# Optimization experiments

Measured on AMD Instinct MI355X. Metric: run time of the kernel, lower is better.

Reference implementation:

```python
import jax, jax.numpy as jnp
import numpy as np
import math

D_MODEL = 1024
D_STATE = 64
DT_MIN, DT_MAX = 1e-3, 1e-1


def setup_inputs() -> dict:
    key = jax.random.key(0)
    ks = jax.random.split(key, 8)
    x = jax.random.normal(ks[0], (2, 4096, D_MODEL), dtype=jnp.float32)
    # in_proj / out_proj: nn.Linear default init (kaiming-uniform-ish); uniform is fine for a reference
    lim = 1.0 / math.sqrt(D_MODEL)
    Win = jax.random.uniform(ks[1], (D_MODEL, D_MODEL), minval=-lim, maxval=lim, dtype=jnp.float32)
    bin_ = jax.random.uniform(ks[2], (D_MODEL,), minval=-lim, maxval=lim, dtype=jnp.float32)
    Wout = jax.random.uniform(ks[3], (D_MODEL, D_MODEL), minval=-lim, maxval=lim, dtype=jnp.float32)
    bout = jax.random.uniform(ks[4], (D_MODEL,), minval=-lim, maxval=lim, dtype=jnp.float32)
    # HiPPO-LegS style init: A_log[d, n] = log(n + 1)
    A_log = jnp.broadcast_to(jnp.log(jnp.arange(1, D_STATE + 1, dtype=jnp.float32)), (D_MODEL, D_STATE))
    B = 0.1 * jax.random.normal(ks[5], (D_MODEL, D_STATE), dtype=jnp.float32)
    C = 0.1 * jax.random.normal(ks[6], (D_MODEL, D_STATE), dtype=jnp.float32)
    Dp = jnp.ones((D_MODEL,), dtype=jnp.float32)
    log_dt = jax.random.uniform(ks[7], (D_MODEL,), dtype=jnp.float32) * (math.log(DT_MAX) - math.log(DT_MIN)) + math.log(DT_MIN)
    dt = jnp.exp(log_dt)
    return {"x": x, "Win": Win, "bin_": bin_, "A_log": A_log, "B": B, "C": C,
            "Dp": Dp, "dt": dt, "Wout": Wout, "bout": bout}


def reference(x, Win, bin_, A_log, B, C, Dp, dt, Wout, bout):
    b, L, d = x.shape
    x = x @ Win.T + bin_                      # in_proj
    u = jnp.transpose(x, (0, 2, 1))           # [b, d, l]
    A = -jnp.exp(-A_log)                      # [d, n], negative real poles
    logdA = A * dt[:, None]                   # log(dA) since dA = exp(A*dt) > 0
    dB = B * dt[:, None]                      # [d, n]
    t = jnp.arange(L, dtype=x.dtype)
    # dA**t == exp(t * log dA): vectorized Vandermonde, replaces per-step power loop
    powers = jnp.exp(logdA[:, :, None] * t)   # [d, n, L]
    k = jnp.einsum('dn,dnl->dl', C * dB, powers)  # SSM conv kernel [d, L]
    n_fft = 2 * L
    k_f = jnp.fft.rfft(k, n=n_fft)            # [d, F]
    u_f = jnp.fft.rfft(u, n=n_fft)            # [b, d, F]
    y = jnp.fft.irfft(u_f * k_f[None], n=n_fft)[..., :L]  # causal conv
    y = y + u * Dp[:, None]                   # skip connection
    y = jnp.transpose(y, (0, 2, 1))           # [b, l, d]
    return y @ Wout.T + bout                  # out_proj
```

## Files before the change

### kernel.cpp

```cpp
#include <hip/hip_runtime.h>
#include <cstdint>
#include <cstddef>

#define D_MODEL 1024
#define D_STATE 64
#define SEQ     4096
#define BATCH   2
#define MROWS   (BATCH*SEQ)

typedef __bf16 bf16x8 __attribute__((ext_vector_type(8)));
typedef float  f32x4  __attribute__((ext_vector_type(4)));
typedef unsigned short u16;
typedef unsigned int   u32;

union BF8 { bf16x8 v; uint4 q; u16 e[8]; };

__device__ __forceinline__ u16 f2bf(float x) {
    u32 u = __float_as_uint(x);
    u32 r = u + 0x7FFFu + ((u >> 16) & 1u);
    return (u16)(r >> 16);
}
__device__ __forceinline__ float bf2f(u16 h) {
    return __uint_as_float(((u32)h) << 16);
}
__device__ __forceinline__ uint4 pack8u(const u16* e) {
    return make_uint4((u32)e[0] | ((u32)e[1] << 16), (u32)e[2] | ((u32)e[3] << 16),
                      (u32)e[4] | ((u32)e[5] << 16), (u32)e[6] | ((u32)e[7] << 16));
}

__device__ __forceinline__ void async16(const void* g, void* l) {
    __builtin_amdgcn_global_load_lds(
        (const __attribute__((address_space(1))) unsigned int*)(uintptr_t)g,
        (__attribute__((address_space(3))) unsigned int*)(uintptr_t)l,
        16, 0, 0);
}

__global__ __launch_bounds__(256) void prep_kernel(
    const float* __restrict__ x, const float* __restrict__ Win,
    const float* __restrict__ Wout,
    u16* __restrict__ Ax, u16* __restrict__ Bw1, u16* __restrict__ Bw2)
{
    const int blk = blockIdx.x, tid = threadIdx.x;
    const int k = tid * 4;
    const float* src; u16* dst; int row;
    if (blk < MROWS)                  { src = x;    dst = Ax;  row = blk; }
    else if (blk < MROWS + D_MODEL)   { src = Win;  dst = Bw1; row = blk - MROWS; }
    else                              { src = Wout; dst = Bw2; row = blk - MROWS - D_MODEL; }
    const float4 v = *reinterpret_cast<const float4*>(src + (size_t)row * D_MODEL + k);
    *reinterpret_cast<uint2*>(dst + (size_t)row * D_MODEL + k) =
        make_uint2((u32)f2bf(v.x) | ((u32)f2bf(v.y) << 16),
                   (u32)f2bf(v.z) | ((u32)f2bf(v.w) << 16));
}

template<int MODE>
__global__ __launch_bounds__(256) void gemm_bt(
    const u16* __restrict__ A, const u16* __restrict__ Bm,
    const float* __restrict__ bias, float* __restrict__ out)
{
    __shared__ u16 As[128 * 64];
    __shared__ u16 Bs[128 * 64];
    __shared__ float Tt[MODE == 1 ? 4 * 16 * 65 : 4];
    const int m0 = blockIdx.y * 128, n0 = blockIdx.x * 128;
    const int tid = threadIdx.x;
    const int wave = tid >> 6, lane = tid & 63;
    const int wm = wave >> 1, wn = wave & 1;
    const int qm = lane & 15, qk = lane >> 4;
    f32x4 acc[4][4] = {};
    for (int k0 = 0; k0 < D_MODEL; k0 += 64) {
        #pragma unroll
        for (int it = 0; it < 4; ++it) {
            const int c   = it * 256 + tid;
            const int row = c >> 3, col = (c & 7) * 8;
            const int ldsbase = (it * 256 + wave * 64) * 8;
            async16(&A[(size_t)(m0 + row) * D_MODEL + k0 + col], &As[ldsbase]);
            async16(&Bm[(size_t)(n0 + row) * D_MODEL + k0 + col], &Bs[ldsbase]);
        }
        __syncthreads();
        #pragma unroll
        for (int kk = 0; kk < 2; ++kk) {
            bf16x8 af[4], bg[4];
            #pragma unroll
            for (int i = 0; i < 4; ++i) {
                af[i] = *reinterpret_cast<const bf16x8*>(&As[(wm*64 + i*16 + qm)*64 + kk*32 + qk*8]);
                bg[i] = *reinterpret_cast<const bf16x8*>(&Bs[(wn*64 + i*16 + qm)*64 + kk*32 + qk*8]);
            }
            #pragma unroll
            for (int i = 0; i < 4; ++i)
                #pragma unroll
                for (int j = 0; j < 4; ++j)
                    acc[i][j] = __builtin_amdgcn_mfma_f32_16x16x32_bf16(af[i], bg[j], acc[i][j], 0, 0, 0);
        }
        __syncthreads();
    }
    if (MODE == 0) {
        #pragma unroll
        for (int i = 0; i < 4; ++i) {
            const int r0 = m0 + wm*64 + i*16 + qk*4;
            #pragma unroll
            for (int j = 0; j < 4; ++j) {
                const int c = n0 + wn*64 + j*16 + qm;
                const float bv = bias[c];
                #pragma unroll
                for (int reg = 0; reg < 4; ++reg)
                    out[(size_t)(r0 + reg) * D_MODEL + c] = acc[i][j][reg] + bv;
            }
        }
    } else {
        float* T = &Tt[wave * 16 * 65];
        float bvj[4];
        #pragma unroll
        for (int j = 0; j < 4; ++j) bvj[j] = bias[n0 + wn*64 + j*16 + qm];
        const int dcol = n0 + wn*64 + lane;
        #pragma unroll
        for (int i = 0; i < 4; ++i) {
            #pragma unroll
            for (int j = 0; j < 4; ++j)
                #pragma unroll
                for (int reg = 0; reg < 4; ++reg)
                    T[(qk*4 + reg) * 65 + j*16 + qm] = acc[i][j][reg] + bvj[j];
            __builtin_amdgcn_wave_barrier();
            float4 o[4];
            #pragma unroll
            for (int t4 = 0; t4 < 4; ++t4)
                o[t4] = make_float4(T[(t4*4 + 0) * 65 + lane], T[(t4*4 + 1) * 65 + lane],
                                    T[(t4*4 + 2) * 65 + lane], T[(t4*4 + 3) * 65 + lane]);
            const int r0 = m0 + wm*64 + i*16;
            const int bb = r0 >> 12, l0 = r0 & (SEQ - 1);
            float* dst = &out[((size_t)(bb * D_MODEL + dcol)) * SEQ + l0];
            #pragma unroll
            for (int t4 = 0; t4 < 4; ++t4)
                reinterpret_cast<float4*>(dst)[t4] = o[t4];
            __builtin_amdgcn_wave_barrier();
        }
    }
}

__global__ __launch_bounds__(128) void scan2_kernel(
    float* __restrict__ ut, const float* __restrict__ A_log,
    const float* __restrict__ Bp, const float* __restrict__ Cp,
    const float* __restrict__ dtp, const float* __restrict__ Dpv)
{
    __shared__ u16 KT_s[64 * 72];
    __shared__ u16 RA_s[64 * 72];
    __shared__ u16 P2_s[64 * 72];
    __shared__ u16 SH[2][64 * 72];
    const int d = blockIdx.x, tid = threadIdx.x;
    const int w = tid >> 6, lane = tid & 63;
    const int qm = lane & 15, qk = lane >> 4;

    const float dt_d  = dtp[d];
    const float logdA = -expf(-A_log[d * D_STATE + lane]) * dt_d;
    const float r     = expf(logdA);
    const float dBn   = Bp[d * D_STATE + lane] * dt_d;
    const float Cv    = Cp[d * D_STATE + lane];
    const float rTn   = expf(logdA * 64.0f);
    const float Dpd   = Dpv[d];

    float* ug = ut + ((size_t)(w * D_MODEL + d)) * SEQ;

    bf16x8 Uf[4][4];
    #pragma unroll
    for (int ct = 0; ct < 4; ++ct) {
        const float* src = ug + (ct * 16 + qm) * 64;
        #pragma unroll
        for (int jb = 0; jb < 2; ++jb) {
            const float4 v0 = *reinterpret_cast<const float4*>(src + jb * 32 + qk * 8);
            const float4 v1 = *reinterpret_cast<const float4*>(src + jb * 32 + qk * 8 + 4);
            const float fv[8] = {v0.x, v0.y, v0.z, v0.w, v1.x, v1.y, v1.z, v1.w};
            BF8 hi, lo;
            #pragma unroll
            for (int i = 0; i < 8; ++i) {
                hi.e[i] = f2bf(fv[i]);
                lo.e[i] = f2bf(fv[i] - bf2f(hi.e[i]));
            }
            Uf[ct][jb]     = hi.v;
            Uf[ct][jb + 2] = lo.v;
        }
    }

    if (w == 1) {
        {
            float p = Cv;
            for (int t = 0; t < 64; ++t) { p *= r; P2_s[t * 72 + lane] = f2bf(p); }
        }
        {
            for (int o = 0; o < 8; ++o) {
                float tmp[8];
                tmp[7] = expf(logdA * (float)(63 - (o * 8 + 7)));
                #pragma unroll
                for (int i = 6; i >= 0; --i) tmp[i] = tmp[i + 1] * r;
                u16 e[8];
                #pragma unroll
                for (int i = 0; i < 8; ++i) e[i] = f2bf(tmp[i]);
                *reinterpret_cast<uint4*>(&RA_s[lane * 72 + o * 8]) = pack8u(e);
            }
        }
    } else {
        float* scr = reinterpret_cast<float*>(&SH[0][0]);
        float* ksh = scr + 64 * 65;
        {
            float p = Cv * dBn;
            for (int m = 0; m < 64; ++m) { scr[m * 65 + lane] = p; p *= r; }
        }
        {
            float kacc = 0.f;
            for (int n = 0; n < 64; ++n) kacc += scr[lane * 65 + n];
            ksh[lane] = kacc;
        }
        {
            for (int o = 0; o < 8; ++o) {
                u16 e[8];
                #pragma unroll
                for (int i = 0; i < 8; ++i) {
                    const int j = o * 8 + i;
                    e[i] = (j <= lane) ? f2bf(ksh[lane - j]) : (u16)0;
                }
                *reinterpret_cast<uint4*>(&KT_s[lane * 72 + o * 8]) = pack8u(e);
            }
        }
    }
    __syncthreads();

    u16* sh = SH[w];
    {
        bf16x8 Af[4][2];
        #pragma unroll
        for (int nt = 0; nt < 4; ++nt)
            #pragma unroll
            for (int jb = 0; jb < 2; ++jb)
                Af[nt][jb] = *reinterpret_cast<const bf16x8*>(
                    &RA_s[(nt * 16 + qm) * 72 + jb * 32 + qk * 8]);
        f32x4 acc[4][4] = {};
        #pragma unroll
        for (int kk = 0; kk < 4; ++kk)
            #pragma unroll
            for (int nt = 0; nt < 4; ++nt)
                #pragma unroll
                for (int ct = 0; ct < 4; ++ct)
                    acc[nt][ct] = __builtin_amdgcn_mfma_f32_16x16x32_bf16(
                        Af[nt][kk & 1], Uf[ct][kk], acc[nt][ct], 0, 0, 0);
        #pragma unroll
        for (int nt = 0; nt < 4; ++nt)
            #pragma unroll
            for (int ct = 0; ct < 4; ++ct) {
                const int c = ct * 16 + qm, nn0 = nt * 16 + qk * 4;
                uint2 pk;
                pk.x = (u32)f2bf(acc[nt][ct][0]) | ((u32)f2bf(acc[nt][ct][1]) << 16);
                pk.y = (u32)f2bf(acc[nt][ct][2]) | ((u32)f2bf(acc[nt][ct][3]) << 16);
                *reinterpret_cast<uint2*>(&sh[c * 72 + nn0]) = pk;
            }
    }
    __syncthreads();

    {
        float h = 0.f;
        for (int c = 0; c < 64; ++c) {
            const float s = bf2f(sh[c * 72 + lane]);
            sh[c * 72 + lane] = f2bf(h);
            h = rTn * h + dBn * s;
        }
    }
    __syncthreads();

    {
        bf16x8 Af[4][2];
        #pragma unroll
        for (int tt = 0; tt < 4; ++tt)
            #pragma unroll
            for (int jb = 0; jb < 2; ++jb)
                Af[tt][jb] = *reinterpret_cast<const bf16x8*>(
                    &KT_s[(tt * 16 + qm) * 72 + jb * 32 + qk * 8]);
        f32x4 acc[4][4] = {};
        #pragma unroll
        for (int kk = 0; kk < 4; ++kk)
            #pragma unroll
            for (int tt = 0; tt < 4; ++tt)
                #pragma unroll
                for (int ct = 0; ct < 4; ++ct)
                    acc[tt][ct] = __builtin_amdgcn_mfma_f32_16x16x32_bf16(
                        Af[tt][kk & 1], Uf[ct][kk], acc[tt][ct], 0, 0, 0);
        bf16x8 Pf[4][2];
        #pragma unroll
        for (int tt = 0; tt < 4; ++tt)
            #pragma unroll
            for (int kb = 0; kb < 2; ++kb)
                Pf[tt][kb] = *reinterpret_cast<const bf16x8*>(
                    &P2_s[(tt * 16 + qm) * 72 + kb * 32 + qk * 8]);
        #pragma unroll
        for (int ct = 0; ct < 4; ++ct)
            #pragma unroll
            for (int kb = 0; kb < 2; ++kb) {
                const bf16x8 Hf = *reinterpret_cast<const bf16x8*>(
                    &sh[(ct * 16 + qm) * 72 + kb * 32 + qk * 8]);
                #pragma unroll
                for (int tt = 0; tt < 4; ++tt)
                    acc[tt][ct] = __builtin_amdgcn_mfma_f32_16x16x32_bf16(
                        Pf[tt][kb], Hf, acc[tt][ct], 0, 0, 0);
            }
        #pragma unroll
        for (int tt = 0; tt < 4; ++tt)
            #pragma unroll
            for (int ct = 0; ct < 4; ++ct) {
                const int c = ct * 16 + qm, t0 = tt * 16 + qk * 4;
                float* dst = ug + c * 64 + t0;
                const float4 u4 = *reinterpret_cast<const float4*>(dst);
                float4 y;
                y.x = acc[tt][ct][0] + Dpd * u4.x;
                y.y = acc[tt][ct][1] + Dpd * u4.y;
                y.z = acc[tt][ct][2] + Dpd * u4.z;
                y.w = acc[tt][ct][3] + Dpd * u4.w;
                *reinterpret_cast<float4*>(dst) = y;
            }
    }
}

__global__ __launch_bounds__(256) void trans_kernel(
    const float* __restrict__ yt, u16* __restrict__ Ax)
{
    __shared__ float T[64 * 68];
    const int b = blockIdx.z, dx = blockIdx.y * 64, lx = blockIdx.x * 64;
    const int tid = threadIdx.x;
    const int t16 = tid >> 4, l16 = tid & 15;
    #pragma unroll
    for (int ii = 0; ii < 4; ++ii) {
        const int dd = ii * 16 + t16;
        const int ll = l16 * 4;
        float4 v = *reinterpret_cast<const float4*>(
            &yt[((size_t)(b * D_MODEL + dx + dd)) * SEQ + lx + ll]);
        *reinterpret_cast<float4*>(&T[dd * 68 + ll]) = v;
    }
    __syncthreads();
    #pragma unroll
    for (int ii = 0; ii < 4; ++ii) {
        const int ll = ii * 16 + t16;
        const int dd = l16 * 4;
        float v0 = T[(dd + 0) * 68 + ll], v1 = T[(dd + 1) * 68 + ll];
        float v2 = T[(dd + 2) * 68 + ll], v3 = T[(dd + 3) * 68 + ll];
        const size_t row = (size_t)b * SEQ + lx + ll;
        *reinterpret_cast<uint2*>(Ax + row * D_MODEL + dx + dd) =
            make_uint2((u32)f2bf(v0) | ((u32)f2bf(v1) << 16),
                       (u32)f2bf(v2) | ((u32)f2bf(v3) << 16));
    }
}

extern "C" void kernel_launch(void* const* d_in, const int* in_sizes, int n_in,
                              void* d_out, int out_size, void* d_ws, size_t ws_size,
                              hipStream_t stream) {
    const float* x     = (const float*)d_in[0];
    const float* Win   = (const float*)d_in[1];
    const float* bin   = (const float*)d_in[2];
    const float* A_log = (const float*)d_in[3];
    const float* Bp    = (const float*)d_in[4];
    const float* Cp    = (const float*)d_in[5];
    const float* Dpv   = (const float*)d_in[6];
    const float* dtp   = (const float*)d_in[7];
    const float* Wout  = (const float*)d_in[8];
    const float* bout  = (const float*)d_in[9];
    float* out = (float*)d_out;

    char* ws = (char*)d_ws;
    u16*   Ax  = (u16*)(ws);
    float* ut  = (float*)(ws + (size_t)25165824);
    u16*   Bw1 = (u16*)(ws + (size_t)58720256);
    u16*   Bw2 = (u16*)(ws + (size_t)60817408);

    prep_kernel<<<MROWS + 2 * D_MODEL, 256, 0, stream>>>(x, Win, Wout, Ax, Bw1, Bw2);
    gemm_bt<1><<<dim3(D_MODEL / 128, MROWS / 128), 256, 0, stream>>>(Ax, Bw1, bin, ut);
    scan2_kernel<<<D_MODEL, 128, 0, stream>>>(ut, A_log, Bp, Cp, dtp, Dpv);
    trans_kernel<<<dim3(SEQ / 64, D_MODEL / 64, BATCH), 256, 0, stream>>>(ut, Ax);
    gemm_bt<0><<<dim3(D_MODEL / 128, MROWS / 128), 256, 0, stream>>>(Ax, Bw2, bout, out);
}
```

Measured before the change: 199.1 us.

## Double-buffer GEMM LDS tiles and restructure SSM kernel precompute

The GEMM now uses two LDS buffers so the async global loads for the next K-slice overlap MFMA work on the current one, with one barrier per slice instead of two. The transpose scratch for MODE 1 reuses the A tile buffer. In the scan kernel, the SSM kernel taps are computed as a dot product of dB with the bf16 power table instead of a 64x65 fp32 scratch, the precompute work is rebalanced across the two waves, and the LDS row stride drops from 72 to 64. The sequential state recurrence batches its LDS reads in groups of 16. Dropping the padding may add LDS bank conflicts, and computing k from bf16 powers costs some precision.

```diff
diff --git a/kernel.cpp b/kernel.cpp
--- a/kernel.cpp
+++ b/kernel.cpp
@@ -57,32 +57,33 @@
     const u16* __restrict__ A, const u16* __restrict__ Bm,
     const float* __restrict__ bias, float* __restrict__ out)
 {
-    __shared__ u16 As[128 * 64];
-    __shared__ u16 Bs[128 * 64];
-    __shared__ float Tt[MODE == 1 ? 4 * 16 * 65 : 4];
+    __shared__ __align__(16) u16 As[2][128 * 64];
+    __shared__ __align__(16) u16 Bs[2][128 * 64];
     const int m0 = blockIdx.y * 128, n0 = blockIdx.x * 128;
     const int tid = threadIdx.x;
     const int wave = tid >> 6, lane = tid & 63;
     const int wm = wave >> 1, wn = wave & 1;
     const int qm = lane & 15, qk = lane >> 4;
     f32x4 acc[4][4] = {};
-    for (int k0 = 0; k0 < D_MODEL; k0 += 64) {
+
+    auto stage = [&](u16* Ad, u16* Bd, int k0) {
         #pragma unroll
         for (int it = 0; it < 4; ++it) {
             const int c   = it * 256 + tid;
             const int row = c >> 3, col = (c & 7) * 8;
             const int ldsbase = (it * 256 + wave * 64) * 8;
-            async16(&A[(size_t)(m0 + row) * D_MODEL + k0 + col], &As[ldsbase]);
-            async16(&Bm[(size_t)(n0 + row) * D_MODEL + k0 + col], &Bs[ldsbase]);
-        }
-        __syncthreads();
+            async16(&A[(size_t)(m0 + row) * D_MODEL + k0 + col], Ad + ldsbase);
+            async16(&Bm[(size_t)(n0 + row) * D_MODEL + k0 + col], Bd + ldsbase);
+        }
+    };
+    auto compute = [&](const u16* As_, const u16* Bs_) {
         #pragma unroll
         for (int kk = 0; kk < 2; ++kk) {
             bf16x8 af[4], bg[4];
             #pragma unroll
             for (int i = 0; i < 4; ++i) {
-                af[i] = *reinterpret_cast<const bf16x8*>(&As[(wm*64 + i*16 + qm)*64 + kk*32 + qk*8]);
-                bg[i] = *reinterpret_cast<const bf16x8*>(&Bs[(wn*64 + i*16 + qm)*64 + kk*32 + qk*8]);
+                af[i] = *reinterpret_cast<const bf16x8*>(&As_[(wm*64 + i*16 + qm)*64 + kk*32 + qk*8]);
+                bg[i] = *reinterpret_cast<const bf16x8*>(&Bs_[(wn*64 + i*16 + qm)*64 + kk*32 + qk*8]);
             }
             #pragma unroll
             for (int i = 0; i < 4; ++i)
@@ -90,8 +91,24 @@
                 for (int j = 0; j < 4; ++j)
                     acc[i][j] = __builtin_amdgcn_mfma_f32_16x16x32_bf16(af[i], bg[j], acc[i][j], 0, 0, 0);
         }
+    };
+
+    stage(As[0], Bs[0], 0);
+    __syncthreads();
+    #pragma unroll 1
+    for (int kp = 0; kp < 7; ++kp) {
+        stage(As[1], Bs[1], 128 * kp + 64);
+        compute(As[0], Bs[0]);
         __syncthreads();
-    }
+        stage(As[0], Bs[0], 128 * kp + 128);
+        compute(As[1], Bs[1]);
+        __syncthreads();
+    }
+    stage(As[1], Bs[1], 960);
+    compute(As[0], Bs[0]);
+    __syncthreads();
+    compute(As[1], Bs[1]);
+
     if (MODE == 0) {
         #pragma unroll
         for (int i = 0; i < 4; ++i) {
@@ -106,6 +123,7 @@
             }
         }
     } else {
+        float* Tt = reinterpret_cast<float*>(&As[0][0]);
         float* T = &Tt[wave * 16 * 65];
         float bvj[4];
         #pragma unroll
@@ -140,10 +158,10 @@
     const float* __restrict__ Bp, const float* __restrict__ Cp,
     const float* __restrict__ dtp, const float* __restrict__ Dpv)
 {
-    __shared__ u16 KT_s[64 * 72];
-    __shared__ u16 RA_s[64 * 72];
-    __shared__ u16 P2_s[64 * 72];
-    __shared__ u16 SH[2][64 * 72];
+    __shared__ __align__(16) u16 KT_s[64 * 64];
+    __shared__ __align__(16) u16 RA_s[64 * 64];
+    __shared__ __align__(16) u16 P2_s[64 * 64];
+    __shared__ __align__(16) u16 SH[2][64 * 64];
     const int d = blockIdx.x, tid = threadIdx.x;
     const int w = tid >> 6, lane = tid & 63;
     const int qm = lane & 15, qk = lane >> 4;
@@ -158,6 +176,10 @@
 
     float* ug = ut + ((size_t)(w * D_MODEL + d)) * SEQ;
 
+    float* dB_sh = reinterpret_cast<float*>(&SH[0][0]);
+    float* w_sh  = dB_sh + 64;
+    float* k_sh  = dB_sh + 128;
+
     bf16x8 Uf[4][4];
     #pragma unroll
     for (int ct = 0; ct < 4; ++ct) {
@@ -178,45 +200,45 @@
         }
     }
 
-    if (w == 1) {
-        {
-            float p = Cv;
-            for (int t = 0; t < 64; ++t) { p *= r; P2_s[t * 72 + lane] = f2bf(p); }
-        }
-        {
+    if (w == 0) {
+        dB_sh[lane] = dBn;
+        w_sh[lane]  = Cv * dBn;
+        for (int o = 0; o < 8; ++o) {
+            float tmp[8];
+            tmp[7] = expf(logdA * (float)(63 - (o * 8 + 7)));
+            #pragma unroll
+            for (int i = 6; i >= 0; --i) tmp[i] = tmp[i + 1] * r;
+            u16 e[8];
+            #pragma unroll
+            for (int i = 0; i < 8; ++i) e[i] = f2bf(tmp[i]);
+            *reinterpret_cast<uint4*>(&RA_s[lane * 64 + o * 8]) = pack8u(e);
+        }
+    } else {
+        float p = Cv;
+        for (int t = 0; t < 64; ++t) { p *= r; P2_s[t * 64 + lane] = f2bf(p); }
+    }
+    __syncthreads();
+    if (w == 0) {
+        float kacc = 0.f;
+        if (lane == 0) {
+            for (int n = 0; n < 64; ++n) kacc += w_sh[n];
+        } else {
+            const u16* prow = &P2_s[(lane - 1) * 64];
             for (int o = 0; o < 8; ++o) {
-                float tmp[8];
-                tmp[7] = expf(logdA * (float)(63 - (o * 8 + 7)));
-                #pragma unroll
-                for (int i = 6; i >= 0; --i) tmp[i] = tmp[i + 1] * r;
-                u16 e[8];
-                #pragma unroll
-                for (int i = 0; i < 8; ++i) e[i] = f2bf(tmp[i]);
-                *reinterpret_cast<uint4*>(&RA_s[lane * 72 + o * 8]) = pack8u(e);
-            }
-        }
-    } else {
-        float* scr = reinterpret_cast<float*>(&SH[0][0]);
-        float* ksh = scr + 64 * 65;
-        {
-            float p = Cv * dBn;
-            for (int m = 0; m < 64; ++m) { scr[m * 65 + lane] = p; p *= r; }
-        }
-        {
-            float kacc = 0.f;
-            for (int n = 0; n < 64; ++n) kacc += scr[lane * 65 + n];
-            ksh[lane] = kacc;
-        }
-        {
-            for (int o = 0; o < 8; ++o) {
-                u16 e[8];
-                #pragma unroll
-                for (int i = 0; i < 8; ++i) {
-                    const int j = o * 8 + i;
-                    e[i] = (j <= lane) ? f2bf(ksh[lane - j]) : (u16)0;
-                }
-                *reinterpret_cast<uint4*>(&KT_s[lane * 72 + o * 8]) = pack8u(e);
-            }
+                BF8 p8; p8.q = *reinterpret_cast<const uint4*>(&prow[o * 8]);
+                #pragma unroll
+                for (int i = 0; i < 8; ++i) kacc += dB_sh[o * 8 + i] * bf2f(p8.e[i]);
+            }
+        }
+        k_sh[lane] = kacc;
+        for (int o = 0; o < 8; ++o) {
+            u16 e[8];
+            #pragma unroll
+            for (int i = 0; i < 8; ++i) {
+                const int j = o * 8 + i;
+                e[i] = (j <= lane) ? f2bf(k_sh[lane - j]) : (u16)0;
+            }
+            *reinterpret_cast<uint4*>(&KT_s[lane * 64 + o * 8]) = pack8u(e);
         }
     }
     __syncthreads();
@@ -229,7 +251,7 @@
             #pragma unroll
             for (int jb = 0; jb < 2; ++jb)
                 Af[nt][jb] = *reinterpret_cast<const bf16x8*>(
-                    &RA_s[(nt * 16 + qm) * 72 + jb * 32 + qk * 8]);
+                    &RA_s[(nt * 16 + qm) * 64 + jb * 32 + qk * 8]);
         f32x4 acc[4][4] = {};
         #pragma unroll
         for (int kk = 0; kk < 4; ++kk)
@@ -247,17 +269,23 @@
                 uint2 pk;
                 pk.x = (u32)f2bf(acc[nt][ct][0]) | ((u32)f2bf(acc[nt][ct][1]) << 16);
                 pk.y = (u32)f2bf(acc[nt][ct][2]) | ((u32)f2bf(acc[nt][ct][3]) << 16);
-                *reinterpret_cast<uint2*>(&sh[c * 72 + nn0]) = pk;
+                *reinterpret_cast<uint2*>(&sh[c * 64 + nn0]) = pk;
             }
     }
     __syncthreads();
 
     {
         float h = 0.f;
-        for (int c = 0; c < 64; ++c) {
-            const float s = bf2f(sh[c * 72 + lane]);
-            sh[c * 72 + lane] = f2bf(h);
-            h = rTn * h + dBn * s;
+        u16* col = sh + lane;
+        for (int b = 0; b < 4; ++b) {
+            float sb[16];
+            #pragma unroll
+            for (int i = 0; i < 16; ++i) sb[i] = bf2f(col[(b * 16 + i) * 64]);
+            #pragma unroll
+            for (int i = 0; i < 16; ++i) {
+                col[(b * 16 + i) * 64] = f2bf(h);
+                h = rTn * h + dBn * sb[i];
+            }
         }
     }
     __syncthreads();
@@ -269,7 +297,7 @@
             #pragma unroll
             for (int jb = 0; jb < 2; ++jb)
                 Af[tt][jb] = *reinterpret_cast<const bf16x8*>(
-                    &KT_s[(tt * 16 + qm) * 72 + jb * 32 + qk * 8]);
+                    &KT_s[(tt * 16 + qm) * 64 + jb * 32 + qk * 8]);
         f32x4 acc[4][4] = {};
         #pragma unroll
         for (int kk = 0; kk < 4; ++kk)
@@ -285,13 +313,13 @@
             #pragma unroll
             for (int kb = 0; kb < 2; ++kb)
                 Pf[tt][kb] = *reinterpret_cast<const bf16x8*>(
-                    &P2_s[(tt * 16 + qm) * 72 + kb * 32 + qk * 8]);
+                    &P2_s[(tt * 16 + qm) * 64 + kb * 32 + qk * 8]);
         #pragma unroll
         for (int ct = 0; ct < 4; ++ct)
             #pragma unroll
             for (int kb = 0; kb < 2; ++kb) {
                 const bf16x8 Hf = *reinterpret_cast<const bf16x8*>(
-                    &sh[(ct * 16 + qm) * 72 + kb * 32 + qk * 8]);
+                    &sh[(ct * 16 + qm) * 64 + kb * 32 + qk * 8]);
                 #pragma unroll
                 for (int tt = 0; tt < 4; ++tt)
                     acc[tt][ct] = __builtin_amdgcn_mfma_f32_16x16x32_bf16(
```

Result: faster. 192.0 us (-3.6%).
